# Kernel optimization log

Measured on AMD Instinct MI355X. Metric: run time of the kernel, lower is better.

Reference implementation:

```python
import math
import jax, jax.numpy as jnp
import numpy as np

B, T = 65536, 34
VOCAB, TOK_DIM, POS_DIM, D_MODEL, FFN_DIM, HEAD_DIM = 14, 2, 3, 5, 2, 5
EPS = 1e-5

def _pos_flat_idx():
    # replicate _build_pos_map: 10 digits, Z_HI, 10 digits, Z_HI, 10 digits, special0, special1
    sources, indices = [], []
    for _ in range(3):
        for i in range(10):
            sources.append(0); indices.append(i)
        sources.append(2); indices.append(len([s for s in sources if s == 2]) - 1)
    # fix: the torch code appends (2,0),(2,1) after first two digit blocks and (1,0),(2,2) after the third
    sources, indices = [], []
    for i in range(10): sources.append(0); indices.append(i)
    sources.append(2); indices.append(0)
    for i in range(10): sources.append(0); indices.append(i)
    sources.append(2); indices.append(1)
    for i in range(10): sources.append(0); indices.append(i)
    sources.append(1); indices.append(0)
    sources.append(2); indices.append(2)
    src = np.array(sources); idx = np.array(indices)
    # table layout: rows 0..9 digit_pos, row 10 z_hi_pos, rows 11..13 special (learned0, learned1, eos)
    offs = np.array([0, 10, 11])
    return offs[src] + idx  # (34,)

POS_FLAT = jnp.asarray(_pos_flat_idx())
CAUSAL = jnp.tril(jnp.ones((T, T), dtype=bool))

def _rms(x, w):
    return x * jax.lax.rsqrt(jnp.mean(x * x, -1, keepdims=True) + EPS) * w

def setup_inputs():
    key = jax.random.key(0)
    ks = jax.random.split(key, 16)
    n = lambda i, shape: jax.random.normal(ks[i], shape, jnp.float32) * 0.5
    return {
        'idx': jax.random.randint(ks[0], (B, T), 0, VOCAB),
        'tok_emb': n(1, (VOCAB, TOK_DIM)),
        'spiral_amp': jnp.float32(1.0),
        'spiral_phase': jnp.float32(0.1),
        'spiral_slope': jnp.float32(1.0 / 9.0),
        'spiral_offset': jnp.float32(0.05),
        'pos_corr_slope': jnp.float32(0.01),
        'pos_corr_intercept': jnp.float32(0.02),
        'z_hi_pos': n(2, (1, POS_DIM)),
        'special_pos': n(3, (2, POS_DIM)),
        'q_w': n(4, (HEAD_DIM, POS_DIM)),
        'v_w': n(5, (HEAD_DIM, TOK_DIM)),
        'out_A': n(6, (HEAD_DIM, 2)),
        'out_B': n(7, (2, D_MODEL)),
        'q_phase': n(8, (1,)),
        'ln1_w': jnp.ones((D_MODEL,), jnp.float32),
        'ln2_w': jnp.ones((D_MODEL,), jnp.float32),
        'lnf_w': jnp.ones((D_MODEL,), jnp.float32),
        'fc1_w': n(9, (FFN_DIM, D_MODEL)),
        'fc1_b': n(10, (FFN_DIM,)),
        'fc2_w': n(11, (D_MODEL, FFN_DIM)),
        'fc2_b': n(12, (D_MODEL,)),
        'head_w': n(13, (TOK_DIM, D_MODEL)),
    }

def reference(idx, tok_emb, spiral_amp, spiral_phase, spiral_slope, spiral_offset,
              pos_corr_slope, pos_corr_intercept, z_hi_pos, special_pos,
              q_w, v_w, out_A, out_B, q_phase, ln1_w, ln2_w, lnf_w,
              fc1_w, fc1_b, fc2_w, fc2_b, head_w):
    # learned spiral digit positions (10, 3)
    i = jnp.arange(10, dtype=jnp.float32)
    angle = 2.0 * math.pi * i / 10.0 + spiral_phase
    base = jnp.stack([spiral_amp * jnp.cos(angle),
                      spiral_amp * jnp.sin(angle),
                      spiral_slope * i + spiral_offset], -1)
    corr = pos_corr_intercept + pos_corr_slope * i
    digit_pos = base * (1.0 + corr)[:, None]
    table = jnp.concatenate([digit_pos, z_hi_pos, special_pos,
                             jnp.zeros((1, POS_DIM), jnp.float32)], 0)  # (14, 3)
    pos = table[POS_FLAT]  # (T, 3)

    tok = tok_emb[idx]  # (B, T, 2)
    x = jnp.concatenate([tok, jnp.broadcast_to(pos, (idx.shape[0], T, POS_DIM))], -1)  # (B,T,5)

    h = _rms(x, ln1_w)
    q = jnp.einsum('btp,dp->btd', h[..., TOK_DIM:], q_w)  # (B,T,5)
    k = q  # q_proj applied to same input for both q and k
    v = jnp.einsum('btp,dp->btd', h[..., :TOK_DIM], v_w)  # (B,T,5)

    # per-head 2D rotation on first 4 dims (HEAD_DIM//2 = 2 pairs), dim 4 unchanged
    c, s = jnp.cos(q_phase[0]), jnp.sin(q_phase[0])
    q0, q1 = q[..., 0:4:2], q[..., 1:4:2]
    q_rot = jnp.concatenate([
        jnp.stack([q0 * c - q1 * s, q0 * s + q1 * c], -1).reshape(q.shape[:-1] + (4,)),
        q[..., 4:]], -1)

    att = jnp.einsum('btd,bsd->bts', q_rot, k) / math.sqrt(HEAD_DIM)
    att = jnp.where(CAUSAL, att, -jnp.inf)
    att = jax.nn.softmax(att, -1)
    out = jnp.einsum('bts,bsd->btd', att, v)  # (B,T,5)

    x = x + (out @ out_A) @ out_B  # low-rank out_proj
    hh = _rms(x, ln2_w)
    x = x + (jax.nn.gelu(hh @ fc1_w.T + fc1_b, approximate=False) @ fc2_w.T + fc2_b)
    x = _rms(x, lnf_w)
    return (x @ head_w.T) @ tok_emb.T  # (B, T, 14)
```

## Files before the change

### kernel.cpp

```cpp
#include <hip/hip_runtime.h>
#include <math.h>

#define T_SEQ 34
#define NTOK 14
#define NE (T_SEQ * NTOK)

__global__ __launch_bounds__(256) void micro_fused_kernel(
    const int* __restrict__ idx,
    const float* __restrict__ tok_emb,
    const float* __restrict__ s_amp, const float* __restrict__ s_phase,
    const float* __restrict__ s_slope, const float* __restrict__ s_offset,
    const float* __restrict__ pc_slope, const float* __restrict__ pc_int,
    const float* __restrict__ z_hi, const float* __restrict__ spec,
    const float* __restrict__ q_w, const float* __restrict__ v_w,
    const float* __restrict__ out_A, const float* __restrict__ out_B,
    const float* __restrict__ q_phase,
    const float* __restrict__ ln1_w, const float* __restrict__ ln2_w,
    const float* __restrict__ lnf_w,
    const float* __restrict__ fc1_w, const float* __restrict__ fc1_b,
    const float* __restrict__ fc2_w, const float* __restrict__ fc2_b,
    const float* __restrict__ head_w,
    float* __restrict__ out, int N)
{
    __shared__ float Xs[NE * 5];
    __shared__ float Qs[NE * 5];
    __shared__ float Ks[NE * 5];
    __shared__ float Vs[NE * 5];
    __shared__ float Ws[5 * NTOK];
    __shared__ float M5s[25];
    __shared__ float ln2s[5], lnfs[5], fc1ws[10], fc1bs[2], fc2ws[10], fc2bs[5];
    __shared__ int toks[9 * T_SEQ];

    const int tid = threadIdx.x;

    {
        const float amp = s_amp[0], ph = s_phase[0], slp = s_slope[0], off = s_offset[0];
        const float pcs = pc_slope[0], pci = pc_int[0];
        const float cph = cosf(q_phase[0]), sph = sinf(q_phase[0]);
        const float invs5 = 0.44721359549995793f;
        for (int e = tid; e < NE; e += 256) {
            int t = e / NTOK, tk = e - t * NTOK;
            float px, py, pz;
            if (t == 33)      { px = 0.f;     py = 0.f;     pz = 0.f; }
            else if (t == 32) { px = z_hi[0]; py = z_hi[1]; pz = z_hi[2]; }
            else if (t == 10) { px = spec[0]; py = spec[1]; pz = spec[2]; }
            else if (t == 21) { px = spec[3]; py = spec[4]; pz = spec[5]; }
            else {
                int i = (t < 10) ? t : (t < 21 ? t - 11 : t - 22);
                float fi = (float)i;
                float ang = 0.62831853071795864769f * fi + ph;
                float mlt = 1.f + pci + pcs * fi;
                px = amp * cosf(ang) * mlt;
                py = amp * sinf(ang) * mlt;
                pz = (slp * fi + off) * mlt;
            }
            float x0 = tok_emb[tk * 2], x1 = tok_emb[tk * 2 + 1];
            float ssum = x0 * x0 + x1 * x1 + px * px + py * py + pz * pz;
            float r = rsqrtf(ssum * 0.2f + 1e-5f);
            float h0 = x0 * r * ln1_w[0], h1 = x1 * r * ln1_w[1];
            float h2 = px * r * ln1_w[2], h3 = py * r * ln1_w[3], h4 = pz * r * ln1_w[4];
            float q0 = q_w[0]  * h2 + q_w[1]  * h3 + q_w[2]  * h4;
            float q1 = q_w[3]  * h2 + q_w[4]  * h3 + q_w[5]  * h4;
            float q2 = q_w[6]  * h2 + q_w[7]  * h3 + q_w[8]  * h4;
            float q3 = q_w[9]  * h2 + q_w[10] * h3 + q_w[11] * h4;
            float q4 = q_w[12] * h2 + q_w[13] * h3 + q_w[14] * h4;
            float* X = &Xs[e * 5]; X[0] = x0; X[1] = x1; X[2] = px; X[3] = py; X[4] = pz;
            float* K = &Ks[e * 5];
            K[0] = q0 * invs5; K[1] = q1 * invs5; K[2] = q2 * invs5;
            K[3] = q3 * invs5; K[4] = q4 * invs5;
            float* Q = &Qs[e * 5];
            Q[0] = q0 * cph - q1 * sph; Q[1] = q0 * sph + q1 * cph;
            Q[2] = q2 * cph - q3 * sph; Q[3] = q2 * sph + q3 * cph; Q[4] = q4;
            float* V = &Vs[e * 5];
            V[0] = v_w[0] * h0 + v_w[1] * h1; V[1] = v_w[2] * h0 + v_w[3] * h1;
            V[2] = v_w[4] * h0 + v_w[5] * h1; V[3] = v_w[6] * h0 + v_w[7] * h1;
            V[4] = v_w[8] * h0 + v_w[9] * h1;
        }
    }
    if (tid < 70) {
        int d = tid / NTOK, v = tid - d * NTOK;
        Ws[tid] = head_w[d] * tok_emb[v * 2] + head_w[5 + d] * tok_emb[v * 2 + 1];
    }
    if (tid < 25) {
        int i = tid / 5, j = tid - i * 5;
        M5s[tid] = out_A[i * 2] * out_B[j] + out_A[i * 2 + 1] * out_B[5 + j];
    }
    if (tid < 5)  { ln2s[tid] = ln2_w[tid]; lnfs[tid] = lnf_w[tid]; fc2bs[tid] = fc2_b[tid]; }
    if (tid < 10) { fc1ws[tid] = fc1_w[tid]; fc2ws[tid] = fc2_w[tid]; }
    if (tid < 2)  { fc1bs[tid] = fc1_b[tid]; }

    const int blockStart = blockIdx.x * 256;
    const int b0 = blockStart / T_SEQ;
    int lastLin = blockStart + 255; if (lastLin >= N) lastLin = N - 1;
    const int nrows = lastLin / T_SEQ - b0 + 1;
    for (int i = tid; i < nrows * T_SEQ; i += 256)
        toks[i] = idx[b0 * T_SEQ + i];

    __syncthreads();

    const int lin = blockStart + tid;
    if (lin >= N) return;
    const int b = lin / T_SEQ;
    const int t = lin - b * T_SEQ;
    const int* row = &toks[(b - b0) * T_SEQ];

    const int et = (t * NTOK + row[t]) * 5;
    float qv[5], xv[5];
#pragma unroll
    for (int d = 0; d < 5; ++d) { qv[d] = Qs[et + d]; xv[d] = Xs[et + d]; }

    float m = -1e30f, l = 0.f;
    float a0 = 0.f, a1 = 0.f, a2 = 0.f, a3 = 0.f, a4 = 0.f;
    int base = 0;
    for (int s = 0; s <= t; ++s, base += 5 * NTOK) {
        int o = base + row[s] * 5;
        float sc = qv[0] * Ks[o]     + qv[1] * Ks[o + 1] + qv[2] * Ks[o + 2]
                 + qv[3] * Ks[o + 3] + qv[4] * Ks[o + 4];
        float nm = fmaxf(m, sc);
        float al = __expf(m - nm);
        float p  = __expf(sc - nm);
        l = l * al + p;
        a0 = a0 * al + p * Vs[o];     a1 = a1 * al + p * Vs[o + 1];
        a2 = a2 * al + p * Vs[o + 2]; a3 = a3 * al + p * Vs[o + 3];
        a4 = a4 * al + p * Vs[o + 4];
        m = nm;
    }
    float il = 1.f / l;
    float o0 = a0 * il, o1 = a1 * il, o2 = a2 * il, o3 = a3 * il, o4 = a4 * il;

    float y[5];
#pragma unroll
    for (int j = 0; j < 5; ++j)
        y[j] = xv[j] + o0 * M5s[j] + o1 * M5s[5 + j] + o2 * M5s[10 + j]
             + o3 * M5s[15 + j] + o4 * M5s[20 + j];

    float s2 = y[0]*y[0] + y[1]*y[1] + y[2]*y[2] + y[3]*y[3] + y[4]*y[4];
    float r2 = rsqrtf(s2 * 0.2f + 1e-5f);
    float hh[5];
#pragma unroll
    for (int j = 0; j < 5; ++j) hh[j] = y[j] * r2 * ln2s[j];

    float u0 = fc1bs[0], u1 = fc1bs[1];
#pragma unroll
    for (int j = 0; j < 5; ++j) { u0 += hh[j] * fc1ws[j]; u1 += hh[j] * fc1ws[5 + j]; }
    float g0 = 0.5f * u0 * (1.f + erff(u0 * 0.70710678118654752f));
    float g1 = 0.5f * u1 * (1.f + erff(u1 * 0.70710678118654752f));

    float y2[5]; float s3 = 0.f;
#pragma unroll
    for (int j = 0; j < 5; ++j) {
        y2[j] = y[j] + g0 * fc2ws[j * 2] + g1 * fc2ws[j * 2 + 1] + fc2bs[j];
        s3 += y2[j] * y2[j];
    }
    float r3 = rsqrtf(s3 * 0.2f + 1e-5f);
    float z[5];
#pragma unroll
    for (int j = 0; j < 5; ++j) z[j] = y2[j] * r3 * lnfs[j];

    float res[14];
#pragma unroll
    for (int v = 0; v < 14; ++v)
        res[v] = z[0] * Ws[v] + z[1] * Ws[14 + v] + z[2] * Ws[28 + v]
               + z[3] * Ws[42 + v] + z[4] * Ws[56 + v];

    float2* op = (float2*)(out + (size_t)lin * 14);
#pragma unroll
    for (int v = 0; v < 7; ++v) op[v] = make_float2(res[2 * v], res[2 * v + 1]);
}

extern "C" void kernel_launch(void* const* d_in, const int* in_sizes, int n_in,
                              void* d_out, int out_size, void* d_ws, size_t ws_size,
                              hipStream_t stream) {
    const int N = in_sizes[0];
    const int grid = (N + 255) / 256;
    micro_fused_kernel<<<grid, 256, 0, stream>>>(
        (const int*)d_in[0],
        (const float*)d_in[1], (const float*)d_in[2], (const float*)d_in[3],
        (const float*)d_in[4], (const float*)d_in[5], (const float*)d_in[6],
        (const float*)d_in[7], (const float*)d_in[8], (const float*)d_in[9],
        (const float*)d_in[10], (const float*)d_in[11], (const float*)d_in[12],
        (const float*)d_in[13], (const float*)d_in[14], (const float*)d_in[15],
        (const float*)d_in[16], (const float*)d_in[17], (const float*)d_in[18],
        (const float*)d_in[19], (const float*)d_in[20], (const float*)d_in[21],
        (const float*)d_in[22],
        (float*)d_out, N);
}
```

Baseline: 259.9 us.

## Fold attention projections algebraically into low-dim query and value vectors

Folds the query/key weights and rotation into a 3-element per-query vector dotted directly with the normalized position features. Folds the value projection into the low-rank output projection, so attention accumulates only two values. It also drops the online softmax max tracking, so each key step needs one exp and far fewer LDS loads (one float4 plus one scalar instead of ten scalars). The exchange is that it relies on scores staying small enough not to overflow exp without max subtraction, and floating-point rounding changes slightly.

New measurement: 229.1 us. 11.8% less time.

```diff
diff --git a/kernel.cpp b/kernel.cpp
--- a/kernel.cpp
+++ b/kernel.cpp
@@ -22,12 +22,12 @@
     const float* __restrict__ head_w,
     float* __restrict__ out, int N)
 {
-    __shared__ float Xs[NE * 5];
-    __shared__ float Qs[NE * 5];
-    __shared__ float Ks[NE * 5];
-    __shared__ float Vs[NE * 5];
+    __shared__ float H8[NE * 8];
+    __shared__ float C3[NE * 4];
+    __shared__ float PosT[T_SEQ * 3];
+    __shared__ float TE[NTOK * 2];
+    __shared__ float PMs[10];
     __shared__ float Ws[5 * NTOK];
-    __shared__ float M5s[25];
     __shared__ float ln2s[5], lnfs[5], fc1ws[10], fc1bs[2], fc2ws[10], fc2bs[5];
     __shared__ int toks[9 * T_SEQ];
 
@@ -54,8 +54,9 @@
                 py = amp * sinf(ang) * mlt;
                 pz = (slp * fi + off) * mlt;
             }
+            if (tk == 0) { PosT[t*3] = px; PosT[t*3+1] = py; PosT[t*3+2] = pz; }
             float x0 = tok_emb[tk * 2], x1 = tok_emb[tk * 2 + 1];
-            float ssum = x0 * x0 + x1 * x1 + px * px + py * py + pz * pz;
+            float ssum = x0*x0 + x1*x1 + px*px + py*py + pz*pz;
             float r = rsqrtf(ssum * 0.2f + 1e-5f);
             float h0 = x0 * r * ln1_w[0], h1 = x1 * r * ln1_w[1];
             float h2 = px * r * ln1_w[2], h3 = py * r * ln1_w[3], h4 = pz * r * ln1_w[4];
@@ -64,26 +65,30 @@
             float q2 = q_w[6]  * h2 + q_w[7]  * h3 + q_w[8]  * h4;
             float q3 = q_w[9]  * h2 + q_w[10] * h3 + q_w[11] * h4;
             float q4 = q_w[12] * h2 + q_w[13] * h3 + q_w[14] * h4;
-            float* X = &Xs[e * 5]; X[0] = x0; X[1] = x1; X[2] = px; X[3] = py; X[4] = pz;
-            float* K = &Ks[e * 5];
-            K[0] = q0 * invs5; K[1] = q1 * invs5; K[2] = q2 * invs5;
-            K[3] = q3 * invs5; K[4] = q4 * invs5;
-            float* Q = &Qs[e * 5];
-            Q[0] = q0 * cph - q1 * sph; Q[1] = q0 * sph + q1 * cph;
-            Q[2] = q2 * cph - q3 * sph; Q[3] = q2 * sph + q3 * cph; Q[4] = q4;
-            float* V = &Vs[e * 5];
-            V[0] = v_w[0] * h0 + v_w[1] * h1; V[1] = v_w[2] * h0 + v_w[3] * h1;
-            V[2] = v_w[4] * h0 + v_w[5] * h1; V[3] = v_w[6] * h0 + v_w[7] * h1;
-            V[4] = v_w[8] * h0 + v_w[9] * h1;
+            float r0 = q0 * cph - q1 * sph, r1 = q0 * sph + q1 * cph;
+            float r2c = q2 * cph - q3 * sph, r3 = q2 * sph + q3 * cph;
+            float c0 = (r0*q_w[0] + r1*q_w[3] + r2c*q_w[6] + r3*q_w[9]  + q4*q_w[12]) * invs5;
+            float c1 = (r0*q_w[1] + r1*q_w[4] + r2c*q_w[7] + r3*q_w[10] + q4*q_w[13]) * invs5;
+            float c2 = (r0*q_w[2] + r1*q_w[5] + r2c*q_w[8] + r3*q_w[11] + q4*q_w[14]) * invs5;
+            float* H = &H8[e * 8];
+            H[0] = h2; H[1] = h3; H[2] = h4; H[3] = h0; H[4] = h1;
+            float* C = &C3[e * 4];
+            C[0] = c0; C[1] = c1; C[2] = c2; C[3] = 0.f;
         }
     }
+    if (tid < 28) TE[tid] = tok_emb[tid];
     if (tid < 70) {
         int d = tid / NTOK, v = tid - d * NTOK;
         Ws[tid] = head_w[d] * tok_emb[v * 2] + head_w[5 + d] * tok_emb[v * 2 + 1];
     }
-    if (tid < 25) {
-        int i = tid / 5, j = tid - i * 5;
-        M5s[tid] = out_A[i * 2] * out_B[j] + out_A[i * 2 + 1] * out_B[5 + j];
+    if (tid < 10) {
+        int j = tid >> 1, c = tid & 1;
+        float acc = 0.f;
+        for (int i = 0; i < 5; ++i) {
+            float m5 = out_A[i*2] * out_B[j] + out_A[i*2+1] * out_B[5 + j];
+            acc += m5 * v_w[i*2 + c];
+        }
+        PMs[tid] = acc;
     }
     if (tid < 5)  { ln2s[tid] = ln2_w[tid]; lnfs[tid] = lnf_w[tid]; fc2bs[tid] = fc2_b[tid]; }
     if (tid < 10) { fc1ws[tid] = fc1_w[tid]; fc2ws[tid] = fc2_w[tid]; }
@@ -102,37 +107,32 @@
     if (lin >= N) return;
     const int b = lin / T_SEQ;
     const int t = lin - b * T_SEQ;
-    const int* row = &toks[(b - b0) * T_SEQ];
+    const int rowBase = (b - b0) * T_SEQ;
 
-    const int et = (t * NTOK + row[t]) * 5;
-    float qv[5], xv[5];
-#pragma unroll
-    for (int d = 0; d < 5; ++d) { qv[d] = Qs[et + d]; xv[d] = Xs[et + d]; }
+    const int tokt = toks[rowBase + t];
+    const float4 c3 = *(const float4*)&C3[(t * NTOK + tokt) * 4];
+    const float xv0 = TE[tokt * 2], xv1 = TE[tokt * 2 + 1];
+    const float xv2 = PosT[t*3], xv3 = PosT[t*3+1], xv4 = PosT[t*3+2];
 
-    float m = -1e30f, l = 0.f;
-    float a0 = 0.f, a1 = 0.f, a2 = 0.f, a3 = 0.f, a4 = 0.f;
-    int base = 0;
-    for (int s = 0; s <= t; ++s, base += 5 * NTOK) {
-        int o = base + row[s] * 5;
-        float sc = qv[0] * Ks[o]     + qv[1] * Ks[o + 1] + qv[2] * Ks[o + 2]
-                 + qv[3] * Ks[o + 3] + qv[4] * Ks[o + 4];
-        float nm = fmaxf(m, sc);
-        float al = __expf(m - nm);
-        float p  = __expf(sc - nm);
-        l = l * al + p;
-        a0 = a0 * al + p * Vs[o];     a1 = a1 * al + p * Vs[o + 1];
-        a2 = a2 * al + p * Vs[o + 2]; a3 = a3 * al + p * Vs[o + 3];
-        a4 = a4 * al + p * Vs[o + 4];
-        m = nm;
+    float l = 0.f, a0 = 0.f, a1 = 0.f;
+    for (int s = 0; s <= t; ++s) {
+        int o = (s * NTOK + toks[rowBase + s]) * 8;
+        float4 h = *(const float4*)&H8[o];
+        float h1 = H8[o + 4];
+        float sc = fmaf(c3.x, h.x, fmaf(c3.y, h.y, c3.z * h.z));
+        float p = __expf(sc);
+        l += p;
+        a0 = fmaf(p, h.w, a0);
+        a1 = fmaf(p, h1, a1);
     }
-    float il = 1.f / l;
-    float o0 = a0 * il, o1 = a1 * il, o2 = a2 * il, o3 = a3 * il, o4 = a4 * il;
+    const float il = 1.f / l;
+    a0 *= il; a1 *= il;
 
     float y[5];
 #pragma unroll
     for (int j = 0; j < 5; ++j)
-        y[j] = xv[j] + o0 * M5s[j] + o1 * M5s[5 + j] + o2 * M5s[10 + j]
-             + o3 * M5s[15 + j] + o4 * M5s[20 + j];
+        y[j] = (j == 0 ? xv0 : j == 1 ? xv1 : j == 2 ? xv2 : j == 3 ? xv3 : xv4)
+             + PMs[j*2] * a0 + PMs[j*2+1] * a1;
 
     float s2 = y[0]*y[0] + y[1]*y[1] + y[2]*y[2] + y[3]*y[3] + y[4]*y[4];
     float r2 = rsqrtf(s2 * 0.2f + 1e-5f);
```
